# Kernel tuning notes

Hardware: AMD Instinct MI355X
Metric: run time of the kernel (lower is better)

Reference implementation:

```python
import jax, jax.numpy as jnp
import numpy as np

IMG_H, IMG_W = 900, 1600
NUM_CLASSES = 10
NUM_CAMS = 6

# pcdet boxes_to_corners_3d corner template (unit box, centered)
CORNER_TEMPLATE = jnp.array(
    [[1, 1, -1], [1, -1, -1], [-1, -1, -1], [-1, 1, -1],
     [1, 1, 1], [1, -1, 1], [-1, -1, 1], [-1, 1, 1]], dtype=jnp.float32) * 0.5


def boxes_to_corners_3d(boxes):
    # boxes: [N,7] = (x,y,z,dx,dy,dz,heading) -> [N,8,3]
    dims = boxes[:, 3:6]
    corners = dims[:, None, :] * CORNER_TEMPLATE  # [N,8,3]
    yaw = boxes[:, 6]
    c, s = jnp.cos(yaw), jnp.sin(yaw)
    z = jnp.zeros_like(c)
    o = jnp.ones_like(c)
    # rotate_points_along_z: points @ [[c,s,0],[-s,c,0],[0,0,1]]
    rot = jnp.stack([c, s, z, -s, c, z, z, z, o], axis=-1).reshape(-1, 3, 3)
    corners = jnp.einsum('nkj,njm->nkm', corners, rot)
    return corners + boxes[:, None, 0:3]


def box_iou(a, b):
    # a: [M,4], b: [K,4] xyxy -> [M,K]
    lt = jnp.maximum(a[:, None, :2], b[None, :, :2])
    rb = jnp.minimum(a[:, None, 2:], b[None, :, 2:])
    wh = jnp.clip(rb - lt, 0.0)
    inter = wh[..., 0] * wh[..., 1]
    area_a = (a[:, 2] - a[:, 0]) * (a[:, 3] - a[:, 1])
    area_b = (b[:, 2] - b[:, 0]) * (b[:, 3] - b[:, 1])
    union = area_a[:, None] + area_b[None, :] - inter
    return jnp.where(union > 0, inter / union, 0.0)


def _project_boxes(pred_boxes, img_aug_matrix, lidar_aug_matrix, lidar2image):
    # batch index 0 (B=1); returns proj [6,N,4] and valid [6,N]
    N = pred_boxes.shape[0]
    corners = boxes_to_corners_3d(pred_boxes).reshape(-1, 3)  # [N*8,3]
    la = lidar_aug_matrix[0]
    pts = corners - la[:3, 3]
    pts = jnp.linalg.inv(la[:3, :3]) @ pts.T  # [3, N*8]
    l2i = lidar2image[0]
    cc = l2i[:, :3, :3] @ pts + l2i[:, :3, 3][:, :, None]  # [6,3,N*8]
    zc = jnp.clip(cc[:, 2, :], 1e-5, 1e5)
    xy = cc[:, :2, :] / zc[:, None, :]
    cc = jnp.concatenate([xy, zc[:, None, :]], axis=1)
    ia = img_aug_matrix[0]
    cc = ia[:, :3, :3] @ cc + ia[:, :3, 3][:, :, None]
    pix = jnp.transpose(cc[:, :2, :], (0, 2, 1))  # [6, N*8, 2]
    # .long() truncation (non-differentiable in original)
    pix = jax.lax.stop_gradient(pix).astype(jnp.int32)
    px = jnp.clip(pix[..., 0], 0, IMG_W)
    py = jnp.clip(pix[..., 1], 0, IMG_H)
    pix = jnp.stack([px, py], -1).reshape(NUM_CAMS, N, 8, 2).astype(pred_boxes.dtype)
    xy1 = pix.min(axis=2)  # [6,N,2]
    xy2 = pix.max(axis=2)
    valid = jnp.all((xy2 - xy1) > 0, axis=-1)  # [6,N]
    proj = jnp.concatenate([xy1, xy2], axis=-1)  # [6,N,4]
    return proj, valid


def setup_inputs() -> dict:
    rng = np.random.default_rng(0)
    N, M = 4096, 6144
    xy = rng.uniform(-40, 40, (N, 2))
    zc = rng.uniform(-1, 1, (N, 1))
    dims = rng.uniform(1.0, 4.0, (N, 3))
    yaw = rng.uniform(0, 2 * np.pi, (N, 1))
    pred_boxes = np.concatenate([xy, zc, dims, yaw], axis=1).astype(np.float32)
    # 6 cameras: pinhole intrinsics + yaw-spaced extrinsics
    K = np.array([[1000., 0., 800.], [0., 1000., 450.], [0., 0., 1.]])
    l2i = np.zeros((1, NUM_CAMS, 4, 4), np.float32)
    for ci, ang in enumerate(np.linspace(0, 2 * np.pi, NUM_CAMS, endpoint=False)):
        fwd = np.array([np.cos(ang), np.sin(ang), 0.])
        right = np.array([np.sin(ang), -np.cos(ang), 0.])
        down = np.array([0., 0., -1.])
        R = np.stack([right, down, fwd], 0)
        l2i[0, ci, :3, :3] = K @ R
        l2i[0, ci, 3, 3] = 1.0
    img_aug_matrix = np.tile(np.eye(4, dtype=np.float32), (1, NUM_CAMS, 1, 1))
    lidar_aug_matrix = np.eye(4, dtype=np.float32)[None]
    cx = rng.uniform(0, IMG_W, M)
    cy = rng.uniform(0, IMG_H, M)
    w = rng.uniform(20, 300, M)
    h = rng.uniform(20, 300, M)
    det_boxes = np.stack([np.clip(cx - w / 2, 0, IMG_W), np.clip(cy - h / 2, 0, IMG_H),
                          np.clip(cx + w / 2, 0, IMG_W), np.clip(cy + h / 2, 0, IMG_H)], 1).astype(np.float32)
    det_labels = rng.integers(1, NUM_CLASSES + 1, M).astype(np.int32)
    det_scores = rng.uniform(0.05, 1.0, M).astype(np.float32)
    det_batch_idx = np.zeros(M, np.int32)
    det_cam_idx = (np.arange(M) % NUM_CAMS).astype(np.int32)
    return {
        'pred_boxes': jnp.asarray(pred_boxes),
        'img_aug_matrix': jnp.asarray(img_aug_matrix),
        'lidar_aug_matrix': jnp.asarray(lidar_aug_matrix),
        'lidar2image': jnp.asarray(l2i),
        'det_boxes': jnp.asarray(det_boxes),
        'det_labels': jnp.asarray(det_labels),
        'det_scores': jnp.asarray(det_scores),
        'det_batch_idx': jnp.asarray(det_batch_idx),
        'det_cam_idx': jnp.asarray(det_cam_idx),
    }


def reference(pred_boxes, img_aug_matrix, lidar_aug_matrix, lidar2image,
              det_boxes, det_labels, det_scores, det_batch_idx, det_cam_idx):
    proj, valid = _project_boxes(pred_boxes, img_aug_matrix, lidar_aug_matrix, lidar2image)
    label_matrix = jax.nn.one_hot(det_labels - 1, NUM_CLASSES, dtype=det_scores.dtype) * det_scores[:, None]
    probs_sum = jnp.zeros((pred_boxes.shape[0], NUM_CLASSES), dtype=det_scores.dtype)
    for c in range(NUM_CAMS):
        mask = ((det_cam_idx == c) & (det_batch_idx == 0)).astype(det_boxes.dtype)
        iou = box_iou(det_boxes, proj[c]) * mask[:, None]  # [M,N]
        probs_sum = probs_sum + (iou.T @ label_matrix) * valid[c][:, None]  # [N,10]
    denom = 1e-5 + valid.astype(probs_sum.dtype).sum(axis=0)
    box_probs_mean = probs_sum / denom[:, None]
    pred_scores = jnp.nan_to_num(jnp.max(box_probs_mean, axis=-1), nan=0.0)
    pred_labels = jnp.argmax(box_probs_mean, axis=-1) + 1
    return pred_labels, pred_scores
```

## Files before the change

kernel.cpp:

```cpp
#include <hip/hip_runtime.h>
#include <cstdint>
#include <climits>

#pragma clang fp contract(off)

#define NCAM 6
#define NCLS 10
#define NKEY 60
#define IMGW 1600
#define IMGH 900

__device__ __forceinline__ int sat_f2i(float f) {
    if (f != f) return 0;
    if (f >= 2147483648.0f) return INT_MAX;
    if (f <= -2147483648.0f) return INT_MIN;
    return (int)f;
}

__global__ __launch_bounds__(256) void prep_kernel(
        const float*  __restrict__ boxes,
        const float*  __restrict__ ia,
        const float*  __restrict__ la,
        const float*  __restrict__ l2i,
        const float4* __restrict__ det_boxes,
        const int*    __restrict__ det_labels,
        const float*  __restrict__ det_scores,
        const int*    __restrict__ det_batch,
        const int*    __restrict__ det_cam,
        float* __restrict__ projW,
        float* __restrict__ slab,
        int*   __restrict__ cnt,
        int N, int M, int PB, int CAPW) {
    int tid = threadIdx.x;

    if ((int)blockIdx.x < PB) {
        int n = blockIdx.x * 256 + tid;
        if (n >= N) return;
        float bx = boxes[n*7+0], by = boxes[n*7+1], bz = boxes[n*7+2];
        float dx = boxes[n*7+3], dy = boxes[n*7+4], dz = boxes[n*7+5];
        float yaw = boxes[n*7+6];
        float c = (float)cos((double)yaw);
        float s = (float)sin((double)yaw);

        float a00=la[0],a01=la[1],a02=la[2],t0=la[3];
        float a10=la[4],a11=la[5],a12=la[6],t1=la[7];
        float a20=la[8],a21=la[9],a22=la[10],t2=la[11];
        float det = a00*(a11*a22-a12*a21) - a01*(a10*a22-a12*a20) + a02*(a10*a21-a11*a20);
        float id = 1.0f/det;
        float r00=(a11*a22-a12*a21)*id, r01=(a02*a21-a01*a22)*id, r02=(a01*a12-a02*a11)*id;
        float r10=(a12*a20-a10*a22)*id, r11=(a00*a22-a02*a20)*id, r12=(a02*a10-a00*a12)*id;
        float r20=(a10*a21-a11*a20)*id, r21=(a01*a20-a00*a21)*id, r22=(a00*a11-a01*a10)*id;

        float PX[8], PY[8], PZ[8];
        #pragma unroll
        for (int k = 0; k < 8; k++) {
            float sx = ((k==0||k==1||k==4||k==5) ?  0.5f : -0.5f) * dx;
            float sy = ((k==0||k==3||k==4||k==7) ?  0.5f : -0.5f) * dy;
            float sz = ((k>=4)                   ?  0.5f : -0.5f) * dz;
            float cx = sx*c - sy*s + bx;
            float cy = sx*s + sy*c + by;
            float cz = sz + bz;
            float ux = cx - t0, uy = cy - t1, uz = cz - t2;
            PX[k] = r00*ux + r01*uy + r02*uz;
            PY[k] = r10*ux + r11*uy + r12*uz;
            PZ[k] = r20*ux + r21*uy + r22*uz;
        }
        for (int cam = 0; cam < NCAM; cam++) {
            const float* L = l2i + cam*16;
            const float* A = ia  + cam*16;
            int minx = INT_MAX, miny = INT_MAX, maxx = INT_MIN, maxy = INT_MIN;
            #pragma unroll
            for (int k = 0; k < 8; k++) {
                float u = L[0]*PX[k] + L[1]*PY[k] + L[2]*PZ[k]  + L[3];
                float v = L[4]*PX[k] + L[5]*PY[k] + L[6]*PZ[k]  + L[7];
                float w = L[8]*PX[k] + L[9]*PY[k] + L[10]*PZ[k] + L[11];
                float zc = fminf(fmaxf(w, 1e-5f), 100000.0f);
                float x = u / zc, y = v / zc;
                float xx = A[0]*x + A[1]*y + A[2]*zc + A[3];
                float yy = A[4]*x + A[5]*y + A[6]*zc + A[7];
                int pxi = sat_f2i(xx); pxi = min(max(pxi, 0), IMGW);
                int pyi = sat_f2i(yy); pyi = min(max(pyi, 0), IMGH);
                minx = min(minx, pxi); maxx = max(maxx, pxi);
                miny = min(miny, pyi); maxy = max(maxy, pyi);
            }
            float x1 = (float)minx, y1 = (float)miny, x2 = (float)maxx, y2 = (float)maxy;
            float validf = ((x2 - x1) > 0.0f && (y2 - y1) > 0.0f) ? 1.0f : 0.0f;
            projW[(cam*6+0)*N + n] = x1;
            projW[(cam*6+1)*N + n] = y1;
            projW[(cam*6+2)*N + n] = x2;
            projW[(cam*6+3)*N + n] = y2;
            projW[(cam*6+4)*N + n] = (x2 - x1) * (y2 - y1);
            projW[(cam*6+5)*N + n] = validf;
        }
        return;
    }

    int k = (int)blockIdx.x - PB;
    int cam = k / NCLS, cls = k % NCLS;
    int w = tid >> 6, lane = tid & 63;
    int per = (M + 3) >> 2;
    int m0 = w * per, m1 = min(m0 + per, M);
    float* base = slab + (size_t)(k * 4 + w) * CAPW * 8;
    int pos = 0;
    for (int c = m0; c < m1; c += 64) {
        int m = c + lane;
        bool pred = false;
        if (m < m1) {
            int dc = det_cam[m], db = det_batch[m], dl = det_labels[m] - 1;
            pred = (db == 0) && (dc == cam) && (dl == cls);
        }
        unsigned long long ball = __ballot(pred);
        if (pred) {
            int p = pos + __popcll(ball & ((1ull << lane) - 1ull));
            float4 b = det_boxes[m];
            float area = (b.z - b.x) * (b.w - b.y);
            float4* o = (float4*)(base + (size_t)p * 8);
            o[0] = b;
            o[1] = make_float4(area, det_scores[m], 0.0f, 0.0f);
        }
        pos += __popcll(ball);
    }
    if (lane == 0) cnt[k * 4 + w] = pos;
}

__global__ __launch_bounds__(256) void main_kernel(
        const float* __restrict__ projW,
        const float* __restrict__ slab,
        const int*   __restrict__ cnt,
        float*       __restrict__ partial,
        int N, int CAPW) {
    int tid = threadIdx.x;
    int k = blockIdx.y;
    int cam = k / NCLS;
    int box = blockIdx.x * 256 + tid;
    int bidx = min(box, N - 1);

    float Px1 = projW[(cam*6+0)*N + bidx];
    float Py1 = projW[(cam*6+1)*N + bidx];
    float Px2 = projW[(cam*6+2)*N + bidx];
    float Py2 = projW[(cam*6+3)*N + bidx];
    float Pa  = projW[(cam*6+4)*N + bidx];
    float Pv  = projW[(cam*6+5)*N + bidx];

    float acc = 0.0f;
    #pragma unroll
    for (int sub = 0; sub < 4; sub++) {
        int nk = cnt[k * 4 + sub];
        const float4* bp = (const float4*)(slab + (size_t)(k * 4 + sub) * CAPW * 8);
        for (int m = 0; m < nk; m++) {
            float4 b = bp[2*m];
            float4 q = bp[2*m+1];
            float ltx = fmaxf(b.x, Px1);
            float lty = fmaxf(b.y, Py1);
            float rbx = fminf(b.z, Px2);
            float rby = fminf(b.w, Py2);
            float iw = fmaxf(rbx - ltx, 0.0f);
            float ih = fmaxf(rby - lty, 0.0f);
            float inter = iw * ih;
            float uni = (q.x + Pa) - inter;
            float r = __fdividef(inter, uni);
            float iou = (uni > 0.0f) ? r : 0.0f;
            acc += iou * q.y;
        }
    }
    if (box < N) partial[(size_t)k * N + box] = acc * Pv;
}

__global__ __launch_bounds__(256) void reduce_kernel(
        const float* __restrict__ partial,
        const float* __restrict__ projW,
        float* __restrict__ out, int N) {
    int n = blockIdx.x * 256 + threadIdx.x;
    if (n >= N) return;
    float p[NCLS];
    #pragma unroll
    for (int c = 0; c < NCLS; c++) p[c] = 0.0f;
    #pragma unroll
    for (int cam = 0; cam < NCAM; cam++)
        #pragma unroll
        for (int c = 0; c < NCLS; c++)
            p[c] += partial[(size_t)(cam * NCLS + c) * N + n];
    float nv = 0.0f;
    #pragma unroll
    for (int cam = 0; cam < NCAM; cam++) nv += projW[(cam*6+5)*N + n];
    float denom = 1e-5f + nv;
    float best = -1e30f; int bk = 0;
    #pragma unroll
    for (int c = 0; c < NCLS; c++) {
        float v = p[c] / denom;
        if (v > best) { best = v; bk = c; }
    }
    out[n]     = (float)(bk + 1);
    out[N + n] = best;
}

extern "C" void kernel_launch(void* const* d_in, const int* in_sizes, int n_in,
                              void* d_out, int out_size, void* d_ws, size_t ws_size,
                              hipStream_t stream) {
    const float*  pred_boxes = (const float*)d_in[0];
    const float*  ia         = (const float*)d_in[1];
    const float*  la         = (const float*)d_in[2];
    const float*  l2i        = (const float*)d_in[3];
    const float4* det_boxes  = (const float4*)d_in[4];
    const int*    det_labels = (const int*)d_in[5];
    const float*  det_scores = (const float*)d_in[6];
    const int*    det_batch  = (const int*)d_in[7];
    const int*    det_cam    = (const int*)d_in[8];
    float* out = (float*)d_out;

    int N = in_sizes[0] / 7;
    int M = in_sizes[4] / 4;
    int PB = (N + 255) / 256;
    int CAPW = (M + 3) / 4;

    char* w = (char*)d_ws;
    float* slab    = (float*)w;
    size_t off = (size_t)NKEY * 4 * CAPW * 8 * 4;
    float* projW   = (float*)(w + off);
    off += (size_t)36 * N * 4;
    float* partial = (float*)(w + off);
    off += (size_t)NKEY * N * 4;
    int*   cnt     = (int*)(w + off);

    prep_kernel<<<PB + NKEY, 256, 0, stream>>>(pred_boxes, ia, la, l2i,
                                               det_boxes, det_labels, det_scores,
                                               det_batch, det_cam,
                                               projW, slab, cnt, N, M, PB, CAPW);
    main_kernel<<<dim3(PB, NKEY), 256, 0, stream>>>(projW, slab, cnt, partial, N, CAPW);
    reduce_kernel<<<PB, 256, 0, stream>>>(partial, projW, out, N);
}
```

Before: 122.1 us.

## Fuse three kernels into one cooperative persistent kernel with grid syncs

Replaces the prep, main and reduce kernel launches with a single cooperative kernel of 512 persistent blocks that loops over the work units of each stage and separates the stages with grid-wide syncs. The aim is to remove the launch gaps and inter-kernel dependency stalls between the three small kernels. In exchange it adds grid-sync overhead and caps concurrency at the fixed grid size, and the cooperative launch requires all 512 blocks to be co-resident.

```diff
diff --git a/kernel.cpp b/kernel.cpp
--- a/kernel.cpp
+++ b/kernel.cpp
@@ -1,14 +1,18 @@
 #include <hip/hip_runtime.h>
+#include <hip/hip_cooperative_groups.h>
 #include <cstdint>
 #include <climits>
 
 #pragma clang fp contract(off)
+
+namespace cg = cooperative_groups;
 
 #define NCAM 6
 #define NCLS 10
 #define NKEY 60
 #define IMGW 1600
 #define IMGH 900
+#define GRID 512
 
 __device__ __forceinline__ int sat_f2i(float f) {
     if (f != f) return 0;
@@ -17,7 +21,7 @@
     return (int)f;
 }
 
-__global__ __launch_bounds__(256) void prep_kernel(
+__global__ __launch_bounds__(256, 2) void fused_coop(
         const float*  __restrict__ boxes,
         const float*  __restrict__ ia,
         const float*  __restrict__ la,
@@ -30,168 +34,168 @@
         float* __restrict__ projW,
         float* __restrict__ slab,
         int*   __restrict__ cnt,
+        float* __restrict__ partial,
+        float* __restrict__ out,
         int N, int M, int PB, int CAPW) {
+    cg::grid_group gg = cg::this_grid();
     int tid = threadIdx.x;
 
-    if ((int)blockIdx.x < PB) {
-        int n = blockIdx.x * 256 + tid;
-        if (n >= N) return;
-        float bx = boxes[n*7+0], by = boxes[n*7+1], bz = boxes[n*7+2];
-        float dx = boxes[n*7+3], dy = boxes[n*7+4], dz = boxes[n*7+5];
-        float yaw = boxes[n*7+6];
-        float c = (float)cos((double)yaw);
-        float s = (float)sin((double)yaw);
-
-        float a00=la[0],a01=la[1],a02=la[2],t0=la[3];
-        float a10=la[4],a11=la[5],a12=la[6],t1=la[7];
-        float a20=la[8],a21=la[9],a22=la[10],t2=la[11];
-        float det = a00*(a11*a22-a12*a21) - a01*(a10*a22-a12*a20) + a02*(a10*a21-a11*a20);
-        float id = 1.0f/det;
-        float r00=(a11*a22-a12*a21)*id, r01=(a02*a21-a01*a22)*id, r02=(a01*a12-a02*a11)*id;
-        float r10=(a12*a20-a10*a22)*id, r11=(a00*a22-a02*a20)*id, r12=(a02*a10-a00*a12)*id;
-        float r20=(a10*a21-a11*a20)*id, r21=(a01*a20-a00*a21)*id, r22=(a00*a11-a01*a10)*id;
-
-        float PX[8], PY[8], PZ[8];
-        #pragma unroll
-        for (int k = 0; k < 8; k++) {
-            float sx = ((k==0||k==1||k==4||k==5) ?  0.5f : -0.5f) * dx;
-            float sy = ((k==0||k==3||k==4||k==7) ?  0.5f : -0.5f) * dy;
-            float sz = ((k>=4)                   ?  0.5f : -0.5f) * dz;
-            float cx = sx*c - sy*s + bx;
-            float cy = sx*s + sy*c + by;
-            float cz = sz + bz;
-            float ux = cx - t0, uy = cy - t1, uz = cz - t2;
-            PX[k] = r00*ux + r01*uy + r02*uz;
-            PY[k] = r10*ux + r11*uy + r12*uz;
-            PZ[k] = r20*ux + r21*uy + r22*uz;
-        }
-        for (int cam = 0; cam < NCAM; cam++) {
-            const float* L = l2i + cam*16;
-            const float* A = ia  + cam*16;
-            int minx = INT_MAX, miny = INT_MAX, maxx = INT_MIN, maxy = INT_MIN;
+    for (int u = blockIdx.x; u < PB + NKEY; u += GRID) {
+        if (u < PB) {
+            int n = u * 256 + tid;
+            if (n >= N) continue;
+            float bx = boxes[n*7+0], by = boxes[n*7+1], bz = boxes[n*7+2];
+            float dx = boxes[n*7+3], dy = boxes[n*7+4], dz = boxes[n*7+5];
+            float yaw = boxes[n*7+6];
+            float c = (float)cos((double)yaw);
+            float s = (float)sin((double)yaw);
+
+            float a00=la[0],a01=la[1],a02=la[2],t0=la[3];
+            float a10=la[4],a11=la[5],a12=la[6],t1=la[7];
+            float a20=la[8],a21=la[9],a22=la[10],t2=la[11];
+            float det = a00*(a11*a22-a12*a21) - a01*(a10*a22-a12*a20) + a02*(a10*a21-a11*a20);
+            float id = 1.0f/det;
+            float r00=(a11*a22-a12*a21)*id, r01=(a02*a21-a01*a22)*id, r02=(a01*a12-a02*a11)*id;
+            float r10=(a12*a20-a10*a22)*id, r11=(a00*a22-a02*a20)*id, r12=(a02*a10-a00*a12)*id;
+            float r20=(a10*a21-a11*a20)*id, r21=(a01*a20-a00*a21)*id, r22=(a00*a11-a01*a10)*id;
+
+            float PX[8], PY[8], PZ[8];
             #pragma unroll
             for (int k = 0; k < 8; k++) {
-                float u = L[0]*PX[k] + L[1]*PY[k] + L[2]*PZ[k]  + L[3];
-                float v = L[4]*PX[k] + L[5]*PY[k] + L[6]*PZ[k]  + L[7];
-                float w = L[8]*PX[k] + L[9]*PY[k] + L[10]*PZ[k] + L[11];
-                float zc = fminf(fmaxf(w, 1e-5f), 100000.0f);
-                float x = u / zc, y = v / zc;
-                float xx = A[0]*x + A[1]*y + A[2]*zc + A[3];
-                float yy = A[4]*x + A[5]*y + A[6]*zc + A[7];
-                int pxi = sat_f2i(xx); pxi = min(max(pxi, 0), IMGW);
-                int pyi = sat_f2i(yy); pyi = min(max(pyi, 0), IMGH);
-                minx = min(minx, pxi); maxx = max(maxx, pxi);
-                miny = min(miny, pyi); maxy = max(maxy, pyi);
-            }
-            float x1 = (float)minx, y1 = (float)miny, x2 = (float)maxx, y2 = (float)maxy;
-            float validf = ((x2 - x1) > 0.0f && (y2 - y1) > 0.0f) ? 1.0f : 0.0f;
-            projW[(cam*6+0)*N + n] = x1;
-            projW[(cam*6+1)*N + n] = y1;
-            projW[(cam*6+2)*N + n] = x2;
-            projW[(cam*6+3)*N + n] = y2;
-            projW[(cam*6+4)*N + n] = (x2 - x1) * (y2 - y1);
-            projW[(cam*6+5)*N + n] = validf;
-        }
-        return;
-    }
-
-    int k = (int)blockIdx.x - PB;
-    int cam = k / NCLS, cls = k % NCLS;
-    int w = tid >> 6, lane = tid & 63;
-    int per = (M + 3) >> 2;
-    int m0 = w * per, m1 = min(m0 + per, M);
-    float* base = slab + (size_t)(k * 4 + w) * CAPW * 8;
-    int pos = 0;
-    for (int c = m0; c < m1; c += 64) {
-        int m = c + lane;
-        bool pred = false;
-        if (m < m1) {
-            int dc = det_cam[m], db = det_batch[m], dl = det_labels[m] - 1;
-            pred = (db == 0) && (dc == cam) && (dl == cls);
-        }
-        unsigned long long ball = __ballot(pred);
-        if (pred) {
-            int p = pos + __popcll(ball & ((1ull << lane) - 1ull));
-            float4 b = det_boxes[m];
-            float area = (b.z - b.x) * (b.w - b.y);
-            float4* o = (float4*)(base + (size_t)p * 8);
-            o[0] = b;
-            o[1] = make_float4(area, det_scores[m], 0.0f, 0.0f);
-        }
-        pos += __popcll(ball);
-    }
-    if (lane == 0) cnt[k * 4 + w] = pos;
-}
-
-__global__ __launch_bounds__(256) void main_kernel(
-        const float* __restrict__ projW,
-        const float* __restrict__ slab,
-        const int*   __restrict__ cnt,
-        float*       __restrict__ partial,
-        int N, int CAPW) {
-    int tid = threadIdx.x;
-    int k = blockIdx.y;
-    int cam = k / NCLS;
-    int box = blockIdx.x * 256 + tid;
-    int bidx = min(box, N - 1);
-
-    float Px1 = projW[(cam*6+0)*N + bidx];
-    float Py1 = projW[(cam*6+1)*N + bidx];
-    float Px2 = projW[(cam*6+2)*N + bidx];
-    float Py2 = projW[(cam*6+3)*N + bidx];
-    float Pa  = projW[(cam*6+4)*N + bidx];
-    float Pv  = projW[(cam*6+5)*N + bidx];
-
-    float acc = 0.0f;
-    #pragma unroll
-    for (int sub = 0; sub < 4; sub++) {
-        int nk = cnt[k * 4 + sub];
-        const float4* bp = (const float4*)(slab + (size_t)(k * 4 + sub) * CAPW * 8);
-        for (int m = 0; m < nk; m++) {
-            float4 b = bp[2*m];
-            float4 q = bp[2*m+1];
-            float ltx = fmaxf(b.x, Px1);
-            float lty = fmaxf(b.y, Py1);
-            float rbx = fminf(b.z, Px2);
-            float rby = fminf(b.w, Py2);
-            float iw = fmaxf(rbx - ltx, 0.0f);
-            float ih = fmaxf(rby - lty, 0.0f);
-            float inter = iw * ih;
-            float uni = (q.x + Pa) - inter;
-            float r = __fdividef(inter, uni);
-            float iou = (uni > 0.0f) ? r : 0.0f;
-            acc += iou * q.y;
+                float sx = ((k==0||k==1||k==4||k==5) ?  0.5f : -0.5f) * dx;
+                float sy = ((k==0||k==3||k==4||k==7) ?  0.5f : -0.5f) * dy;
+                float sz = ((k>=4)                   ?  0.5f : -0.5f) * dz;
+                float cx = sx*c - sy*s + bx;
+                float cy = sx*s + sy*c + by;
+                float cz = sz + bz;
+                float ux = cx - t0, uy = cy - t1, uz = cz - t2;
+                PX[k] = r00*ux + r01*uy + r02*uz;
+                PY[k] = r10*ux + r11*uy + r12*uz;
+                PZ[k] = r20*ux + r21*uy + r22*uz;
+            }
+            for (int cam = 0; cam < NCAM; cam++) {
+                const float* L = l2i + cam*16;
+                const float* A = ia  + cam*16;
+                int minx = INT_MAX, miny = INT_MAX, maxx = INT_MIN, maxy = INT_MIN;
+                #pragma unroll
+                for (int k = 0; k < 8; k++) {
+                    float u3 = L[0]*PX[k] + L[1]*PY[k] + L[2]*PZ[k]  + L[3];
+                    float v3 = L[4]*PX[k] + L[5]*PY[k] + L[6]*PZ[k]  + L[7];
+                    float w3 = L[8]*PX[k] + L[9]*PY[k] + L[10]*PZ[k] + L[11];
+                    float zc = fminf(fmaxf(w3, 1e-5f), 100000.0f);
+                    float x = u3 / zc, y = v3 / zc;
+                    float xx = A[0]*x + A[1]*y + A[2]*zc + A[3];
+                    float yy = A[4]*x + A[5]*y + A[6]*zc + A[7];
+                    int pxi = sat_f2i(xx); pxi = min(max(pxi, 0), IMGW);
+                    int pyi = sat_f2i(yy); pyi = min(max(pyi, 0), IMGH);
+                    minx = min(minx, pxi); maxx = max(maxx, pxi);
+                    miny = min(miny, pyi); maxy = max(maxy, pyi);
+                }
+                float x1 = (float)minx, y1 = (float)miny, x2 = (float)maxx, y2 = (float)maxy;
+                float validf = ((x2 - x1) > 0.0f && (y2 - y1) > 0.0f) ? 1.0f : 0.0f;
+                projW[(cam*6+0)*N + n] = x1;
+                projW[(cam*6+1)*N + n] = y1;
+                projW[(cam*6+2)*N + n] = x2;
+                projW[(cam*6+3)*N + n] = y2;
+                projW[(cam*6+4)*N + n] = (x2 - x1) * (y2 - y1);
+                projW[(cam*6+5)*N + n] = validf;
+            }
+        } else {
+            int k = u - PB;
+            int cam = k / NCLS, cls = k % NCLS;
+            int w = tid >> 6, lane = tid & 63;
+            int per = (M + 3) >> 2;
+            int m0 = w * per, m1 = min(m0 + per, M);
+            float* sb = slab + (size_t)(k * 4 + w) * CAPW * 8;
+            int pos = 0;
+            for (int c = m0; c < m1; c += 64) {
+                int m = c + lane;
+                bool pred = false;
+                if (m < m1) {
+                    int dc = det_cam[m], db = det_batch[m], dl = det_labels[m] - 1;
+                    pred = (db == 0) && (dc == cam) && (dl == cls);
+                }
+                unsigned long long ball = __ballot(pred);
+                if (pred) {
+                    int p = pos + __popcll(ball & ((1ull << lane) - 1ull));
+                    float4 b = det_boxes[m];
+                    float area = (b.z - b.x) * (b.w - b.y);
+                    float4* o = (float4*)(sb + (size_t)p * 8);
+                    o[0] = b;
+                    o[1] = make_float4(area, det_scores[m], 0.0f, 0.0f);
+                }
+                pos += __popcll(ball);
+            }
+            if (lane == 0) cnt[k * 4 + w] = pos;
         }
     }
-    if (box < N) partial[(size_t)k * N + box] = acc * Pv;
-}
-
-__global__ __launch_bounds__(256) void reduce_kernel(
-        const float* __restrict__ partial,
-        const float* __restrict__ projW,
-        float* __restrict__ out, int N) {
-    int n = blockIdx.x * 256 + threadIdx.x;
-    if (n >= N) return;
-    float p[NCLS];
-    #pragma unroll
-    for (int c = 0; c < NCLS; c++) p[c] = 0.0f;
-    #pragma unroll
-    for (int cam = 0; cam < NCAM; cam++)
-        #pragma unroll
-        for (int c = 0; c < NCLS; c++)
-            p[c] += partial[(size_t)(cam * NCLS + c) * N + n];
-    float nv = 0.0f;
-    #pragma unroll
-    for (int cam = 0; cam < NCAM; cam++) nv += projW[(cam*6+5)*N + n];
-    float denom = 1e-5f + nv;
-    float best = -1e30f; int bk = 0;
-    #pragma unroll
-    for (int c = 0; c < NCLS; c++) {
-        float v = p[c] / denom;
-        if (v > best) { best = v; bk = c; }
+
+    gg.sync();
+
+    for (int u = blockIdx.x; u < PB * NKEY; u += GRID) {
+        int k = u / PB;
+        int bx = u - k * PB;
+        int cam = k / NCLS;
+        int box = bx * 256 + tid;
+        int bidx = min(box, N - 1);
+
+        float Px1 = projW[(cam*6+0)*N + bidx];
+        float Py1 = projW[(cam*6+1)*N + bidx];
+        float Px2 = projW[(cam*6+2)*N + bidx];
+        float Py2 = projW[(cam*6+3)*N + bidx];
+        float Pa  = projW[(cam*6+4)*N + bidx];
+        float Pv  = projW[(cam*6+5)*N + bidx];
+
+        float acc = 0.0f;
+        #pragma unroll
+        for (int sub = 0; sub < 4; sub++) {
+            int nk = cnt[k * 4 + sub];
+            const float4* bp = (const float4*)(slab + (size_t)(k * 4 + sub) * CAPW * 8);
+            for (int m = 0; m < nk; m++) {
+                float4 b = bp[2*m];
+                float4 q = bp[2*m+1];
+                float ltx = fmaxf(b.x, Px1);
+                float lty = fmaxf(b.y, Py1);
+                float rbx = fminf(b.z, Px2);
+                float rby = fminf(b.w, Py2);
+                float iw = fmaxf(rbx - ltx, 0.0f);
+                float ih = fmaxf(rby - lty, 0.0f);
+                float inter = iw * ih;
+                float uni = (q.x + Pa) - inter;
+                float r = __fdividef(inter, uni);
+                float iou = (uni > 0.0f) ? r : 0.0f;
+                acc += iou * q.y;
+            }
+        }
+        if (box < N) partial[(size_t)k * N + box] = acc * Pv;
     }
-    out[n]     = (float)(bk + 1);
-    out[N + n] = best;
+
+    gg.sync();
+
+    for (int u = blockIdx.x; u < PB; u += GRID) {
+        int n = u * 256 + tid;
+        if (n >= N) continue;
+        float p[NCLS];
+        #pragma unroll
+        for (int c = 0; c < NCLS; c++) p[c] = 0.0f;
+        #pragma unroll
+        for (int cam = 0; cam < NCAM; cam++)
+            #pragma unroll
+            for (int c = 0; c < NCLS; c++)
+                p[c] += partial[(size_t)(cam * NCLS + c) * N + n];
+        float nv = 0.0f;
+        #pragma unroll
+        for (int cam = 0; cam < NCAM; cam++) nv += projW[(cam*6+5)*N + n];
+        float denom = 1e-5f + nv;
+        float best = -1e30f; int bk = 0;
+        #pragma unroll
+        for (int c = 0; c < NCLS; c++) {
+            float v = p[c] / denom;
+            if (v > best) { best = v; bk = c; }
+        }
+        out[n]     = (float)(bk + 1);
+        out[N + n] = best;
+    }
 }
 
 extern "C" void kernel_launch(void* const* d_in, const int* in_sizes, int n_in,
@@ -222,10 +226,13 @@
     off += (size_t)NKEY * N * 4;
     int*   cnt     = (int*)(w + off);
 
-    prep_kernel<<<PB + NKEY, 256, 0, stream>>>(pred_boxes, ia, la, l2i,
-                                               det_boxes, det_labels, det_scores,
-                                               det_batch, det_cam,
-                                               projW, slab, cnt, N, M, PB, CAPW);
-    main_kernel<<<dim3(PB, NKEY), 256, 0, stream>>>(projW, slab, cnt, partial, N, CAPW);
-    reduce_kernel<<<PB, 256, 0, stream>>>(partial, projW, out, N);
+    void* args[] = {
+        (void*)&pred_boxes, (void*)&ia, (void*)&la, (void*)&l2i,
+        (void*)&det_boxes, (void*)&det_labels, (void*)&det_scores,
+        (void*)&det_batch, (void*)&det_cam,
+        (void*)&projW, (void*)&slab, (void*)&cnt, (void*)&partial,
+        (void*)&out, (void*)&N, (void*)&M, (void*)&PB, (void*)&CAPW
+    };
+    hipLaunchCooperativeKernel((const void*)fused_coop, dim3(GRID), dim3(256),
+                               args, 0, stream);
 }
```

After: 255.7 us. +109.4%, slower.

## Register-tile four boxes per thread and stage detections through shared memory

Applied to the files above, without the earlier changes.

The main IoU kernel now has each thread handle four predicted boxes, and each block stages chunks of detection boxes, areas and scores into LDS before looping over them. This amortizes every detection load across four boxes and replaces repeated global/L1 reads with shared-memory broadcasts. FP contraction is enabled in this kernel so multiply-adds can fuse. The cost is fewer blocks in the grid, which lowers parallelism when N is small, plus extra block barriers; fused multiply-adds may also change rounding slightly.

```diff
diff --git a/kernel.cpp b/kernel.cpp
--- a/kernel.cpp
+++ b/kernel.cpp
@@ -9,6 +9,8 @@
 #define NKEY 60
 #define IMGW 1600
 #define IMGH 900
+#define TBOX 4
+#define CHUNK 512
 
 __device__ __forceinline__ int sat_f2i(float f) {
     if (f != f) return 0;
@@ -129,41 +131,69 @@
         const int*   __restrict__ cnt,
         float*       __restrict__ partial,
         int N, int CAPW) {
+    #pragma clang fp contract(fast)
     int tid = threadIdx.x;
     int k = blockIdx.y;
     int cam = k / NCLS;
-    int box = blockIdx.x * 256 + tid;
-    int bidx = min(box, N - 1);
-
-    float Px1 = projW[(cam*6+0)*N + bidx];
-    float Py1 = projW[(cam*6+1)*N + bidx];
-    float Px2 = projW[(cam*6+2)*N + bidx];
-    float Py2 = projW[(cam*6+3)*N + bidx];
-    float Pa  = projW[(cam*6+4)*N + bidx];
-    float Pv  = projW[(cam*6+5)*N + bidx];
-
-    float acc = 0.0f;
+    int box0 = blockIdx.x * (256 * TBOX) + tid;
+
+    __shared__ float4 sbox[CHUNK];
+    __shared__ float2 sq[CHUNK];
+
+    float Px1[TBOX], Py1[TBOX], Px2[TBOX], Py2[TBOX], Pa[TBOX], Pv[TBOX], acc[TBOX];
+    #pragma unroll
+    for (int t = 0; t < TBOX; t++) {
+        int b = box0 + t * 256;
+        int bi = min(b, N - 1);
+        Px1[t] = projW[(cam*6+0)*N + bi];
+        Py1[t] = projW[(cam*6+1)*N + bi];
+        Px2[t] = projW[(cam*6+2)*N + bi];
+        Py2[t] = projW[(cam*6+3)*N + bi];
+        Pa[t]  = projW[(cam*6+4)*N + bi];
+        Pv[t]  = projW[(cam*6+5)*N + bi];
+        acc[t] = 0.0f;
+    }
+
     #pragma unroll
     for (int sub = 0; sub < 4; sub++) {
         int nk = cnt[k * 4 + sub];
-        const float4* bp = (const float4*)(slab + (size_t)(k * 4 + sub) * CAPW * 8);
-        for (int m = 0; m < nk; m++) {
-            float4 b = bp[2*m];
-            float4 q = bp[2*m+1];
-            float ltx = fmaxf(b.x, Px1);
-            float lty = fmaxf(b.y, Py1);
-            float rbx = fminf(b.z, Px2);
-            float rby = fminf(b.w, Py2);
-            float iw = fmaxf(rbx - ltx, 0.0f);
-            float ih = fmaxf(rby - lty, 0.0f);
-            float inter = iw * ih;
-            float uni = (q.x + Pa) - inter;
-            float r = __fdividef(inter, uni);
-            float iou = (uni > 0.0f) ? r : 0.0f;
-            acc += iou * q.y;
-        }
-    }
-    if (box < N) partial[(size_t)k * N + box] = acc * Pv;
+        const float4* gb = (const float4*)(slab + (size_t)(k * 4 + sub) * CAPW * 8);
+        for (int base = 0; base < nk; base += CHUNK) {
+            int cc = min(CHUNK, nk - base);
+            __syncthreads();
+            for (int i = tid; i < cc; i += 256) {
+                float4 b0 = gb[(size_t)(base + i) * 2];
+                float4 b1 = gb[(size_t)(base + i) * 2 + 1];
+                sbox[i] = b0;
+                sq[i] = make_float2(b1.x, b1.y);
+            }
+            __syncthreads();
+            for (int m = 0; m < cc; m++) {
+                float4 b = sbox[m];
+                float2 q = sq[m];
+                #pragma unroll
+                for (int t = 0; t < TBOX; t++) {
+                    float ltx = fmaxf(b.x, Px1[t]);
+                    float lty = fmaxf(b.y, Py1[t]);
+                    float rbx = fminf(b.z, Px2[t]);
+                    float rby = fminf(b.w, Py2[t]);
+                    float iw = fmaxf(rbx - ltx, 0.0f);
+                    float ih = fmaxf(rby - lty, 0.0f);
+                    float inter = iw * ih;
+                    float uni = (q.x + Pa[t]) - inter;
+                    float r = __fdividef(inter, uni);
+                    float iou = (uni > 0.0f) ? r : 0.0f;
+                    acc[t] += iou * q.y;
+                }
+            }
+        }
+    }
+
+    #pragma unroll
+    for (int t = 0; t < TBOX; t++) {
+        int b = box0 + t * 256;
+        if (b < N) partial[(size_t)k * N + b] = acc[t] * Pv[t];
+    }
 }
 
 __global__ __launch_bounds__(256) void reduce_kernel(
@@ -211,6 +241,7 @@
     int N = in_sizes[0] / 7;
     int M = in_sizes[4] / 4;
     int PB = (N + 255) / 256;
+    int BX = (N + 256*TBOX - 1) / (256*TBOX);
     int CAPW = (M + 3) / 4;
 
     char* w = (char*)d_ws;
@@ -226,6 +257,6 @@
                                                det_boxes, det_labels, det_scores,
                                                det_batch, det_cam,
                                                projW, slab, cnt, N, M, PB, CAPW);
-    main_kernel<<<dim3(PB, NKEY), 256, 0, stream>>>(projW, slab, cnt, partial, N, CAPW);
+    main_kernel<<<dim3(BX, NKEY), 256, 0, stream>>>(projW, slab, cnt, partial, N, CAPW);
     reduce_kernel<<<PB, 256, 0, stream>>>(partial, projW, out, N);
 }
```

New measurement: 119.9 us. About the same (-1.8%).
